# Optimization experiments

Measured on AMD Instinct MI355X. Metric: run time of the kernel, lower is better.

## Reference

```python
import jax, jax.numpy as jnp
import numpy as np

HIDDEN = 2048
KEY = 2048
EPS = 1e-05


def setup_inputs() -> dict:
    key = jax.random.key(0)
    k1, k2, k3 = jax.random.split(key, 3)
    B, S = 4, 2048
    x = jax.random.normal(k1, (B, S, HIDDEN), dtype=jnp.float32)
    # kaiming_uniform_ bound for fan_in=HIDDEN (a=sqrt(5) default): sqrt(6/((1+5)*fan_in)) = 1/sqrt(fan_in)
    bq = 1.0 / np.sqrt(HIDDEN)
    qkv = jax.random.uniform(k2, (HIDDEN, KEY * 3), minval=-bq, maxval=bq, dtype=jnp.float32)
    bo = 1.0 / np.sqrt(KEY)
    o_proj = jax.random.uniform(k3, (KEY, HIDDEN), minval=-bo, maxval=bo, dtype=jnp.float32)
    gamma = jnp.ones((HIDDEN,), dtype=jnp.float32)
    beta = jnp.zeros((HIDDEN,), dtype=jnp.float32)
    return {"x": x, "qkv": qkv, "o_proj": o_proj, "gamma": gamma, "beta": beta}


def reference(x, qkv, o_proj, gamma, beta):
    residual = x
    # LayerNorm over last dim
    mu = jnp.mean(x, axis=-1, keepdims=True)
    var = jnp.mean((x - mu) ** 2, axis=-1, keepdims=True)
    x_norm = (x - mu) / jnp.sqrt(var + EPS) * gamma + beta
    q = x_norm @ qkv[:, :KEY]          # [B,S,K]
    k = x_norm @ qkv[:, KEY:2 * KEY]   # [B,S,K]
    v = x_norm @ qkv[:, 2 * KEY:]      # [B,S,K]
    scale = 1.0 / jnp.sqrt(jnp.float32(KEY))
    scores = jnp.einsum('bsk,btk->bst', q, k) * scale  # [B,S,S]
    S_len = x.shape[1]
    causal = jnp.tril(jnp.ones((S_len, S_len), dtype=bool))
    scores = jnp.where(causal[None], scores, -jnp.inf)
    attn = jax.nn.softmax(scores, axis=-1)
    out = attn @ v          # [B,S,K]
    out = out @ o_proj      # [B,S,H]
    return out + residual
```

## Files before the change

### kernel.cpp

```cpp
#include <hip/hip_runtime.h>
#include <stdint.h>

typedef short short8 __attribute__((ext_vector_type(8)));
typedef unsigned short ushort8 __attribute__((ext_vector_type(8)));
typedef float f32x4 __attribute__((ext_vector_type(4)));

#define HD 2048
#define S_LEN 2048
#define NROWS 8192
#define N3 6144

typedef __attribute__((address_space(3))) void lds_void_t;
typedef __attribute__((address_space(1))) void g_void_t;

__device__ inline void gload_lds16(const void* g, void* l) {
    __builtin_amdgcn_global_load_lds((g_void_t*)g, (lds_void_t*)l, 16, 0, 0);
}

__device__ inline unsigned short f2bf(float f) {
    unsigned u = __float_as_uint(f);
    unsigned r = (u + 0x7FFFu + ((u >> 16) & 1u)) >> 16;
    return (unsigned short)r;
}
__device__ inline float bf2f(unsigned short h) {
    return __uint_as_float(((unsigned)h) << 16);
}

__global__ __launch_bounds__(256) void ln_kernel(const float* __restrict__ x,
    const float* __restrict__ gamma, const float* __restrict__ beta,
    unsigned short* __restrict__ xn) {
    int row = blockIdx.x;
    const float* xr = x + (size_t)row * HD;
    int tid = threadIdx.x;
    float v[8];
    float4 a = *(const float4*)(xr + tid * 8);
    float4 b = *(const float4*)(xr + tid * 8 + 4);
    v[0]=a.x; v[1]=a.y; v[2]=a.z; v[3]=a.w; v[4]=b.x; v[5]=b.y; v[6]=b.z; v[7]=b.w;
    float s = 0.f, ss = 0.f;
#pragma unroll
    for (int e = 0; e < 8; e++) { s += v[e]; ss += v[e] * v[e]; }
    for (int off = 32; off > 0; off >>= 1) {
        s += __shfl_down(s, off);
        ss += __shfl_down(ss, off);
    }
    __shared__ float red[10];
    int wave = tid >> 6, lane = tid & 63;
    if (lane == 0) { red[wave] = s; red[4 + wave] = ss; }
    __syncthreads();
    if (tid == 0) {
        float S = red[0] + red[1] + red[2] + red[3];
        float SS = red[4] + red[5] + red[6] + red[7];
        float mu = S * (1.0f / HD);
        float var = SS * (1.0f / HD) - mu * mu;
        red[8] = mu;
        red[9] = rsqrtf(var + 1e-5f);
    }
    __syncthreads();
    float mu = red[8], rstd = red[9];
#pragma unroll
    for (int e = 0; e < 8; e++) {
        int c = tid * 8 + e;
        float val = (v[e] - mu) * rstd * gamma[c] + beta[c];
        xn[(size_t)row * HD + c] = f2bf(val);
    }
}

__global__ __launch_bounds__(256) void transp_f32_bf16(const float* __restrict__ src, int ld_s,
    unsigned short* __restrict__ dst, int ld_d) {
    __shared__ float tile[32][33];
    int c0 = blockIdx.x * 32, r0 = blockIdx.y * 32;
    int tc = threadIdx.x & 31, tr = threadIdx.x >> 5;
#pragma unroll
    for (int i = 0; i < 32; i += 8)
        tile[tr + i][tc] = src[(size_t)(r0 + tr + i) * ld_s + c0 + tc];
    __syncthreads();
#pragma unroll
    for (int i = 0; i < 32; i += 8)
        dst[(size_t)(c0 + tr + i) * ld_d + r0 + tc] = f2bf(tile[tc][tr + i]);
}

__global__ __launch_bounds__(256) void transp_bf16(const unsigned short* __restrict__ src0, int ld_s, long sSz,
    unsigned short* __restrict__ dst0, int ld_d, long sDz) {
    const unsigned short* src = src0 + (size_t)blockIdx.z * sSz;
    unsigned short* dst = dst0 + (size_t)blockIdx.z * sDz;
    __shared__ unsigned short tile[32][33];
    int c0 = blockIdx.x * 32, r0 = blockIdx.y * 32;
    int tc = threadIdx.x & 31, tr = threadIdx.x >> 5;
#pragma unroll
    for (int i = 0; i < 32; i += 8)
        tile[tr + i][tc] = src[(size_t)(r0 + tr + i) * ld_s + c0 + tc];
    __syncthreads();
#pragma unroll
    for (int i = 0; i < 32; i += 8)
        dst[(size_t)(c0 + tr + i) * ld_d + r0 + tc] = tile[tc][tr + i];
}

__global__ __launch_bounds__(256) void softmax_causal(unsigned short* __restrict__ sc) {
    int r = blockIdx.x;
    int s = r & (S_LEN - 1);
    unsigned short* row = sc + (size_t)r * S_LEN;
    int tid = threadIdx.x;
    ushort8 u = *(const ushort8*)(row + tid * 8);
    float v[8];
    float mx = -3.0e38f;
#pragma unroll
    for (int e = 0; e < 8; e++) {
        int t = tid * 8 + e;
        float f = bf2f(u[e]);
        v[e] = (t <= s) ? f : -3.0e38f;
        mx = fmaxf(mx, v[e]);
    }
    for (int off = 32; off > 0; off >>= 1) mx = fmaxf(mx, __shfl_down(mx, off));
    __shared__ float red[8];
    int wave = tid >> 6, lane = tid & 63;
    if (lane == 0) red[wave] = mx;
    __syncthreads();
    mx = fmaxf(fmaxf(red[0], red[1]), fmaxf(red[2], red[3]));
    float ex[8];
    float sum = 0.f;
#pragma unroll
    for (int e = 0; e < 8; e++) {
        ex[e] = (v[e] > -1.0e38f) ? __expf(v[e] - mx) : 0.f;
        sum += ex[e];
    }
    for (int off = 32; off > 0; off >>= 1) sum += __shfl_down(sum, off);
    if (lane == 0) red[4 + wave] = sum;
    __syncthreads();
    float inv = 1.0f / (red[4] + red[5] + red[6] + red[7]);
#pragma unroll
    for (int e = 0; e < 8; e++) {
        row[tid * 8 + e] = f2bf(ex[e] * inv);
    }
}

template <int EPI>
__global__ __launch_bounds__(256) void gemm_nt(
    const unsigned short* __restrict__ Ab, int lda, long sAz,
    const unsigned short* __restrict__ Bb, int ldb, long sBz,
    void* __restrict__ Cb, int ldc, long sCz,
    int kdim, int causal, float scale, const float* __restrict__ resid) {
    int bx = blockIdx.x, by = blockIdx.y, bz = blockIdx.z;
    if (causal == 1 && bx > by) return;
    const unsigned short* A = Ab + (size_t)bz * sAz;
    const unsigned short* Bt = Bb + (size_t)bz * sBz;
    int kmax = kdim;
    if (causal == 2) { int km = (by + 1) * 128; if (km < kmax) kmax = km; }
    int m0 = by * 128, n0 = bx * 128;

    __shared__ unsigned short lA[128 * 32];
    __shared__ unsigned short lB[128 * 32];

    int tid = threadIdx.x;
    int wave = tid >> 6, lane = tid & 63;
    int quad = lane >> 4, l16 = lane & 15;
    int wr = wave >> 1, wc = wave & 1;

    int rs = wave * 32 + (lane >> 2);
    int ck = (lane & 3) * 8;
    const unsigned short* gA0 = A + (size_t)(m0 + rs) * lda + ck;
    const unsigned short* gA1 = gA0 + (size_t)16 * lda;
    const unsigned short* gB0 = Bt + (size_t)(n0 + rs) * ldb + ck;
    const unsigned short* gB1 = gB0 + (size_t)16 * ldb;
    unsigned short* lA0 = &lA[(wave * 2 + 0) * 512];
    unsigned short* lA1 = &lA[(wave * 2 + 1) * 512];
    unsigned short* lB0 = &lB[(wave * 2 + 0) * 512];
    unsigned short* lB1 = &lB[(wave * 2 + 1) * 512];

    f32x4 acc[4][4] = {};

    for (int k0 = 0; k0 < kmax; k0 += 32) {
        __syncthreads();
        gload_lds16(gA0 + k0, lA0);
        gload_lds16(gA1 + k0, lA1);
        gload_lds16(gB0 + k0, lB0);
        gload_lds16(gB1 + k0, lB1);
        __syncthreads();
        short8 af[4], bfr[4];
#pragma unroll
        for (int i = 0; i < 4; i++)
            af[i] = *(const short8*)&lA[(wr * 64 + i * 16 + l16) * 32 + quad * 8];
#pragma unroll
        for (int j = 0; j < 4; j++)
            bfr[j] = *(const short8*)&lB[(wc * 64 + j * 16 + l16) * 32 + quad * 8];
#pragma unroll
        for (int i = 0; i < 4; i++)
#pragma unroll
            for (int j = 0; j < 4; j++)
                acc[i][j] = __builtin_amdgcn_mfma_f32_16x16x32_bf16(af[i], bfr[j], acc[i][j], 0, 0, 0);
    }

    int row0 = m0 + wr * 64 + quad * 4;
    int col0 = n0 + wc * 64 + l16;
    if (EPI == 0 || EPI == 1) {
        unsigned short* C = (unsigned short*)Cb + (size_t)bz * sCz;
#pragma unroll
        for (int i = 0; i < 4; i++)
#pragma unroll
            for (int r = 0; r < 4; r++) {
                int row = row0 + i * 16 + r;
#pragma unroll
                for (int j = 0; j < 4; j++) {
                    float v = acc[i][j][r];
                    if (EPI == 1) v *= scale;
                    C[(size_t)row * ldc + col0 + j * 16] = f2bf(v);
                }
            }
    } else {
        float* C = (float*)Cb + (size_t)bz * sCz;
#pragma unroll
        for (int i = 0; i < 4; i++)
#pragma unroll
            for (int r = 0; r < 4; r++) {
                int row = row0 + i * 16 + r;
#pragma unroll
                for (int j = 0; j < 4; j++) {
                    int col = col0 + j * 16;
                    C[(size_t)row * ldc + col] = acc[i][j][r] + resid[(size_t)row * ldc + col];
                }
            }
    }
}

extern "C" void kernel_launch(void* const* d_in, const int* in_sizes, int n_in,
                              void* d_out, int out_size, void* d_ws, size_t ws_size,
                              hipStream_t stream) {
    const float* x      = (const float*)d_in[0];
    const float* qkv    = (const float*)d_in[1];
    const float* o_proj = (const float*)d_in[2];
    const float* gamma  = (const float*)d_in[3];
    const float* beta   = (const float*)d_in[4];
    float* out = (float*)d_out;

    char* w = (char*)d_ws;
    unsigned short* xn      = (unsigned short*)(w);
    unsigned short* w_t     = (unsigned short*)(w + 33554432);
    unsigned short* o_t     = (unsigned short*)(w + 58720256);
    unsigned short* qkv_out = (unsigned short*)(w + 67108864);
    unsigned short* v_t     = (unsigned short*)(w + 167772160);
    unsigned short* scores  = xn;

    ln_kernel<<<NROWS, 256, 0, stream>>>(x, gamma, beta, xn);
    transp_f32_bf16<<<dim3(192, 64), 256, 0, stream>>>(qkv, N3, w_t, HD);
    transp_f32_bf16<<<dim3(64, 64), 256, 0, stream>>>(o_proj, HD, o_t, HD);
    gemm_nt<0><<<dim3(48, 64, 1), 256, 0, stream>>>(xn, HD, 0L, w_t, HD, 0L,
        (void*)qkv_out, N3, 0L, HD, 0, 1.0f, nullptr);
    transp_bf16<<<dim3(64, 64, 4), 256, 0, stream>>>(qkv_out + 4096, N3, (long)S_LEN * N3,
        v_t, S_LEN, (long)HD * S_LEN);
    float scale = 0.022097086912079608f;
    gemm_nt<1><<<dim3(16, 16, 4), 256, 0, stream>>>(qkv_out, N3, (long)S_LEN * N3,
        qkv_out + 2048, N3, (long)S_LEN * N3,
        (void*)scores, S_LEN, (long)S_LEN * S_LEN, HD, 1, scale, nullptr);
    softmax_causal<<<NROWS, 256, 0, stream>>>(scores);
    gemm_nt<0><<<dim3(16, 16, 4), 256, 0, stream>>>(scores, S_LEN, (long)S_LEN * S_LEN,
        v_t, S_LEN, (long)HD * S_LEN,
        (void*)qkv_out, N3, (long)S_LEN * N3, S_LEN, 2, 1.0f, nullptr);
    gemm_nt<2><<<dim3(16, 64, 1), 256, 0, stream>>>(qkv_out, N3, 0L, o_t, HD, 0L,
        (void*)out, HD, 0L, HD, 0, 1.0f, x);
}
```

Measured before the change: 754.3 us.

## Fuse V transpose into QKV GEMM epilogue, double K-step, reverse causal block order

The QKV projection GEMM now writes the V slice directly in transposed layout from its epilogue, which removes the separate bf16 transpose kernel and its extra global round trip. The GEMM main loop processes 64 K elements per iteration using two 32-wide LDS halves, halving barrier count per K. Causal GEMMs remap blockIdx.y so the heaviest lower rows are scheduled first, for better load balance. The costs are more LDS per block and transposed V stores that are 8-byte scattered writes.

```diff
diff --git a/kernel.cpp b/kernel.cpp
--- a/kernel.cpp
+++ b/kernel.cpp
@@ -3,6 +3,7 @@
 
 typedef short short8 __attribute__((ext_vector_type(8)));
 typedef unsigned short ushort8 __attribute__((ext_vector_type(8)));
+typedef unsigned short ushort4v __attribute__((ext_vector_type(4)));
 typedef float f32x4 __attribute__((ext_vector_type(4)));
 
 #define HD 2048
@@ -79,22 +80,6 @@
         dst[(size_t)(c0 + tr + i) * ld_d + r0 + tc] = f2bf(tile[tc][tr + i]);
 }
 
-__global__ __launch_bounds__(256) void transp_bf16(const unsigned short* __restrict__ src0, int ld_s, long sSz,
-    unsigned short* __restrict__ dst0, int ld_d, long sDz) {
-    const unsigned short* src = src0 + (size_t)blockIdx.z * sSz;
-    unsigned short* dst = dst0 + (size_t)blockIdx.z * sDz;
-    __shared__ unsigned short tile[32][33];
-    int c0 = blockIdx.x * 32, r0 = blockIdx.y * 32;
-    int tc = threadIdx.x & 31, tr = threadIdx.x >> 5;
-#pragma unroll
-    for (int i = 0; i < 32; i += 8)
-        tile[tr + i][tc] = src[(size_t)(r0 + tr + i) * ld_s + c0 + tc];
-    __syncthreads();
-#pragma unroll
-    for (int i = 0; i < 32; i += 8)
-        dst[(size_t)(c0 + tr + i) * ld_d + r0 + tc] = tile[tc][tr + i];
-}
-
 __global__ __launch_bounds__(256) void softmax_causal(unsigned short* __restrict__ sc) {
     int r = blockIdx.x;
     int s = r & (S_LEN - 1);
@@ -138,8 +123,10 @@
     const unsigned short* __restrict__ Ab, int lda, long sAz,
     const unsigned short* __restrict__ Bb, int ldb, long sBz,
     void* __restrict__ Cb, int ldc, long sCz,
-    int kdim, int causal, float scale, const float* __restrict__ resid) {
+    int kdim, int causal, float scale, const float* __restrict__ resid,
+    unsigned short* __restrict__ vt) {
     int bx = blockIdx.x, by = blockIdx.y, bz = blockIdx.z;
+    if (causal) by = gridDim.y - 1 - by;
     if (causal == 1 && bx > by) return;
     const unsigned short* A = Ab + (size_t)bz * sAz;
     const unsigned short* Bt = Bb + (size_t)bz * sBz;
@@ -147,51 +134,81 @@
     if (causal == 2) { int km = (by + 1) * 128; if (km < kmax) kmax = km; }
     int m0 = by * 128, n0 = bx * 128;
 
-    __shared__ unsigned short lA[128 * 32];
-    __shared__ unsigned short lB[128 * 32];
+    __shared__ unsigned short lA[128 * 64];
+    __shared__ unsigned short lB[128 * 64];
 
     int tid = threadIdx.x;
     int wave = tid >> 6, lane = tid & 63;
     int quad = lane >> 4, l16 = lane & 15;
     int wr = wave >> 1, wc = wave & 1;
 
-    int rs = wave * 32 + (lane >> 2);
+    int rstage = wave * 32 + (lane >> 2);
     int ck = (lane & 3) * 8;
-    const unsigned short* gA0 = A + (size_t)(m0 + rs) * lda + ck;
-    const unsigned short* gA1 = gA0 + (size_t)16 * lda;
-    const unsigned short* gB0 = Bt + (size_t)(n0 + rs) * ldb + ck;
-    const unsigned short* gB1 = gB0 + (size_t)16 * ldb;
-    unsigned short* lA0 = &lA[(wave * 2 + 0) * 512];
-    unsigned short* lA1 = &lA[(wave * 2 + 1) * 512];
-    unsigned short* lB0 = &lB[(wave * 2 + 0) * 512];
-    unsigned short* lB1 = &lB[(wave * 2 + 1) * 512];
+    const unsigned short* gA[2][2];
+    const unsigned short* gB[2][2];
+    unsigned short* ldA[2][2];
+    unsigned short* ldB[2][2];
+#pragma unroll
+    for (int r16 = 0; r16 < 2; r16++)
+#pragma unroll
+        for (int h = 0; h < 2; h++) {
+            gA[r16][h] = A + (size_t)(m0 + rstage + r16 * 16) * lda + h * 32 + ck;
+            gB[r16][h] = Bt + (size_t)(n0 + rstage + r16 * 16) * ldb + h * 32 + ck;
+            ldA[r16][h] = &lA[h * 4096 + (wave * 32 + r16 * 16) * 32];
+            ldB[r16][h] = &lB[h * 4096 + (wave * 32 + r16 * 16) * 32];
+        }
 
     f32x4 acc[4][4] = {};
 
-    for (int k0 = 0; k0 < kmax; k0 += 32) {
+    for (int k0 = 0; k0 < kmax; k0 += 64) {
         __syncthreads();
-        gload_lds16(gA0 + k0, lA0);
-        gload_lds16(gA1 + k0, lA1);
-        gload_lds16(gB0 + k0, lB0);
-        gload_lds16(gB1 + k0, lB1);
+#pragma unroll
+        for (int r16 = 0; r16 < 2; r16++)
+#pragma unroll
+            for (int h = 0; h < 2; h++) {
+                gload_lds16(gA[r16][h], ldA[r16][h]);
+                gload_lds16(gB[r16][h], ldB[r16][h]);
+            }
         __syncthreads();
-        short8 af[4], bfr[4];
-#pragma unroll
-        for (int i = 0; i < 4; i++)
-            af[i] = *(const short8*)&lA[(wr * 64 + i * 16 + l16) * 32 + quad * 8];
-#pragma unroll
-        for (int j = 0; j < 4; j++)
-            bfr[j] = *(const short8*)&lB[(wc * 64 + j * 16 + l16) * 32 + quad * 8];
-#pragma unroll
-        for (int i = 0; i < 4; i++)
+#pragma unroll
+        for (int h = 0; h < 2; h++) {
+            short8 af[4], bfr[4];
+#pragma unroll
+            for (int i = 0; i < 4; i++)
+                af[i] = *(const short8*)&lA[h * 4096 + (wr * 64 + i * 16 + l16) * 32 + quad * 8];
 #pragma unroll
             for (int j = 0; j < 4; j++)
-                acc[i][j] = __builtin_amdgcn_mfma_f32_16x16x32_bf16(af[i], bfr[j], acc[i][j], 0, 0, 0);
+                bfr[j] = *(const short8*)&lB[h * 4096 + (wc * 64 + j * 16 + l16) * 32 + quad * 8];
+#pragma unroll
+            for (int i = 0; i < 4; i++)
+#pragma unroll
+                for (int j = 0; j < 4; j++)
+                    acc[i][j] = __builtin_amdgcn_mfma_f32_16x16x32_bf16(af[i], bfr[j], acc[i][j], 0, 0, 0);
+        }
+#pragma unroll
+        for (int r16 = 0; r16 < 2; r16++)
+#pragma unroll
+            for (int h = 0; h < 2; h++) { gA[r16][h] += 64; gB[r16][h] += 64; }
     }
 
     int row0 = m0 + wr * 64 + quad * 4;
     int col0 = n0 + wc * 64 + l16;
-    if (EPI == 0 || EPI == 1) {
+    if (EPI == 3 && n0 >= 4096) {
+        int batch = m0 >> 11;
+        int sl0 = (m0 & 2047) + wr * 64 + quad * 4;
+#pragma unroll
+        for (int j = 0; j < 4; j++) {
+            int kcol = (n0 - 4096) + wc * 64 + j * 16 + l16;
+            unsigned short* base = vt + (size_t)batch * S_LEN * S_LEN + (size_t)kcol * S_LEN + sl0;
+#pragma unroll
+            for (int i = 0; i < 4; i++) {
+                ushort4v p;
+#pragma unroll
+                for (int r = 0; r < 4; r++) p[r] = f2bf(acc[i][j][r]);
+                *(ushort4v*)(base + i * 16) = p;
+            }
+        }
+    } else if (EPI == 0 || EPI == 1 || EPI == 3) {
         unsigned short* C = (unsigned short*)Cb + (size_t)bz * sCz;
 #pragma unroll
         for (int i = 0; i < 4; i++)
@@ -242,18 +259,16 @@
     ln_kernel<<<NROWS, 256, 0, stream>>>(x, gamma, beta, xn);
     transp_f32_bf16<<<dim3(192, 64), 256, 0, stream>>>(qkv, N3, w_t, HD);
     transp_f32_bf16<<<dim3(64, 64), 256, 0, stream>>>(o_proj, HD, o_t, HD);
-    gemm_nt<0><<<dim3(48, 64, 1), 256, 0, stream>>>(xn, HD, 0L, w_t, HD, 0L,
-        (void*)qkv_out, N3, 0L, HD, 0, 1.0f, nullptr);
-    transp_bf16<<<dim3(64, 64, 4), 256, 0, stream>>>(qkv_out + 4096, N3, (long)S_LEN * N3,
-        v_t, S_LEN, (long)HD * S_LEN);
+    gemm_nt<3><<<dim3(48, 64, 1), 256, 0, stream>>>(xn, HD, 0L, w_t, HD, 0L,
+        (void*)qkv_out, N3, 0L, HD, 0, 1.0f, nullptr, v_t);
     float scale = 0.022097086912079608f;
     gemm_nt<1><<<dim3(16, 16, 4), 256, 0, stream>>>(qkv_out, N3, (long)S_LEN * N3,
         qkv_out + 2048, N3, (long)S_LEN * N3,
-        (void*)scores, S_LEN, (long)S_LEN * S_LEN, HD, 1, scale, nullptr);
+        (void*)scores, S_LEN, (long)S_LEN * S_LEN, HD, 1, scale, nullptr, nullptr);
     softmax_causal<<<NROWS, 256, 0, stream>>>(scores);
     gemm_nt<0><<<dim3(16, 16, 4), 256, 0, stream>>>(scores, S_LEN, (long)S_LEN * S_LEN,
         v_t, S_LEN, (long)HD * S_LEN,
-        (void*)qkv_out, N3, (long)S_LEN * N3, S_LEN, 2, 1.0f, nullptr);
+        (void*)qkv_out, N3, (long)S_LEN * N3, S_LEN, 2, 1.0f, nullptr, nullptr);
     gemm_nt<2><<<dim3(16, 64, 1), 256, 0, stream>>>(qkv_out, N3, 0L, o_t, HD, 0L,
-        (void*)out, HD, 0L, HD, 0, 1.0f, x);
-}
+        (void*)out, HD, 0L, HD, 0, 1.0f, x, nullptr);
+}
```

After: 660.4 us. 12.5% less time.
